# Kernel tuning notes

Measured on AMD Instinct MI355X. Metric: run time of the kernel, lower is better.

## Reference

```python
import jax, jax.numpy as jnp
import numpy as np

NF = 16            # num_frequencies
S = 2              # scale_factor
MAX_STD = 0.5
POS_LIMIT = 1.0


def setup_inputs() -> dict:
    key = jax.random.key(0)
    ks = jax.random.split(key, 8)
    B, G, H, W = 16, 256, 128, 128
    hidden, base = 1024, 256
    in_dim = (G + 2 * NF + 1) * S * S  # 4624
    # xavier-uniform-like scales
    lim1 = float(np.sqrt(6.0 / (hidden + in_dim)))
    lim2 = float(np.sqrt(6.0 / (base + hidden)))
    return {
        "position": jax.random.uniform(ks[0], (B, 4), dtype=jnp.float32),
        "gestalt": jax.random.normal(ks[1], (B, G), dtype=jnp.float32),
        "mask": jax.random.uniform(ks[2], (B, 1, H, W), dtype=jnp.float32),
        "depth": jax.random.normal(ks[3], (B, 1, H, W), dtype=jnp.float32),
        "weight1": jax.random.uniform(ks[4], (hidden, in_dim), minval=-lim1, maxval=lim1, dtype=jnp.float32),
        "bias1": jnp.zeros((hidden,), dtype=jnp.float32),
        "weight2": jax.random.uniform(ks[5], (base, hidden), minval=-lim2, maxval=lim2, dtype=jnp.float32),
        "bias2": jnp.zeros((base,), dtype=jnp.float32),
    }


def reference(position, gestalt, mask, depth, weight1, bias1, weight2, bias2):
    B, _, H, W = mask.shape
    # positional grids in [-1, 1], shapes (1,1,H,W)
    gx = (jnp.arange(W, dtype=jnp.float32) / (W - 1)) * 2 - 1
    gy = (jnp.arange(H, dtype=jnp.float32) / (H - 1)) * 2 - 1
    grid_y, grid_x = jnp.meshgrid(gy, gx, indexing="ij")
    grid_x = grid_x[None, None]
    grid_y = grid_y[None, None]

    x = jnp.clip(position[:, 0], -POS_LIMIT, POS_LIMIT)[:, None, None, None]
    y = jnp.clip(position[:, 1], -POS_LIMIT, POS_LIMIT)[:, None, None, None]
    min_std = 1.0 / min(H, W)
    std = 0.1 / jnp.clip(position[:, 3], min_std, MAX_STD)[:, None, None, None]
    std_y = std
    std_x = std * (W / H)

    half_pi = jnp.float32(np.pi / 2)
    ngx = (grid_x - x) * std_x * half_pi  # (B,1,H,W)
    ngy = (grid_y - y) * std_y * half_pi
    freqs = (2.0 ** jnp.arange(NF, dtype=jnp.float32))[None, :, None, None]
    cos_x = jnp.cos(ngx * freqs)  # (B,NF,H,W)
    cos_y = jnp.cos(ngy * freqs)
    # interleave: [cx0, cy0, cx1, cy1, ...]
    embedding = jnp.stack([cos_x, cos_y], axis=2).reshape(B, 2 * NF, H, W)

    inp = jnp.concatenate(
        [gestalt[:, :, None, None] * mask, embedding * mask, depth * mask], axis=1
    )  # (B,C,H,W)
    C = inp.shape[1]
    # space-to-depth patchify
    p = inp.reshape(B, C, H // S, S, W // S, S)
    p = p.transpose(0, 2, 4, 1, 3, 5).reshape(B * (H // S) * (W // S), C * S * S)

    h = p @ weight1.T + bias1
    h = h * jax.nn.sigmoid(h)  # SiLU
    o = h @ weight2.T + bias2
    return o.reshape(B, H // S, W // S, -1).transpose(0, 3, 1, 2)
```

## Files before the change

kernel.cpp:

```cpp
#include <hip/hip_runtime.h>
#include <cstdio>


#define NFREQ 16
#define BB 16
#define G 256
#define KIN 1156
#define K1 144
#define STAGE_U16 12800
#define NSTAGE 6

typedef unsigned short u16;
using bf16x8 = __bf16 __attribute__((ext_vector_type(8)));
using f32x16 = float __attribute__((ext_vector_type(16)));
using f32x4  = float __attribute__((ext_vector_type(4)));

__device__ __forceinline__ u16 f2bf(float f) {
  unsigned u = __float_as_uint(f);
  u += 0x7fffu + ((u >> 16) & 1u);
  return (u16)(u >> 16);
}
__device__ __forceinline__ unsigned pk2(float a, float b) {
  return (unsigned)f2bf(a) | ((unsigned)f2bf(b) << 16);
}
__device__ __forceinline__ unsigned pk2f(float a, float b) {
  unsigned ua = __float_as_uint(a) + 0x8000u;
  unsigned ub = __float_as_uint(b) + 0x8000u;
  return __builtin_amdgcn_perm(ub, ua, 0x07060302u);
}
__device__ __forceinline__ float silu(float h) {
  float e = __builtin_amdgcn_exp2f(h * -1.44269504088896f);
  return h * __builtin_amdgcn_rcpf(1.f + e);
}
__device__ __forceinline__ void gl_lds16(const u16* g, u16* l) {
  __builtin_amdgcn_global_load_lds(
      (const __attribute__((address_space(1))) void*)g,
      (__attribute__((address_space(3))) void*)l, 16, 0, 0);
}

__global__ void k_pre(const float* __restrict__ pos,
                      const float* __restrict__ gestalt,
                      const float* __restrict__ w1,
                      const float* __restrict__ w2,
                      const float* __restrict__ bias1,
                      float* __restrict__ cosx, float* __restrict__ cosy,
                      u16* __restrict__ B1F, u16* __restrict__ W2F) {
  const int bid = blockIdx.x;
  const int t = threadIdx.x;

  if (bid < 1024) {
    __shared__ float w1row[KIN];
    __shared__ float gestT[G * 17];
    __shared__ float psum[256];
    __shared__ float wg[64];
    const int n = bid;
    const float b1v = bias1[n];
#pragma unroll
    for (int i = t; i < KIN; i += 256) w1row[i] = w1[(size_t)n * KIN + i];
#pragma unroll
    for (int i = t; i < BB * G; i += 256) {
      int bb = i >> 8, c = i & 255;
      gestT[c * 17 + bb] = gestalt[i];
    }
    __syncthreads();
    {
      int bb = t & 15, j = (t >> 4) & 3, q = t >> 6;
      float acc = 0.f;
#pragma unroll 8
      for (int c = q * 64; c < q * 64 + 64; ++c)
        acc += gestT[c * 17 + bb] * w1row[4 * c + j];
      psum[t] = acc;
    }
    __syncthreads();
    if (t < 64) {
      int bb = t >> 2, j = t & 3;
      wg[t] = psum[j * 16 + bb] + psum[64 + j * 16 + bb] +
              psum[128 + j * 16 + bb] + psum[192 + j * 16 + bb];
    }
    __syncthreads();
    const int ch = n >> 5, l31n = n & 31;
    for (int c = t; c < BB * (K1 / 8); c += 256) {
      int bb = c / 18, kc = c - bb * 18;
      int k0 = kc * 8;
      float v[8];
#pragma unroll
      for (int i = 0; i < 8; ++i) {
        int k = k0 + i;
        float vv;
        if (k < 64)       vv = w1row[1024 + 8 * (k >> 2) + (k & 3)];
        else if (k < 128) { int kk = k - 64; vv = w1row[1024 + 8 * (kk >> 2) + 4 + (kk & 3)]; }
        else if (k < 132) vv = wg[bb * 4 + (k - 128)];
        else if (k < 136) vv = w1row[1152 + (k - 132)];
        else if (k == 136) vv = b1v;
        else              vv = 0.f;
        v[i] = vv;
      }
      uint4 u;
      u.x = pk2(v[0], v[1]); u.y = pk2(v[2], v[3]);
      u.z = pk2(v[4], v[5]); u.w = pk2(v[6], v[7]);
      size_t idx0 = ((((size_t)bb * 32 + ch) * 9 + (kc >> 1)) * 64 +
                     (kc & 1) * 32 + l31n) * 8;
      *(uint4*)(B1F + idx0) = u;
    }
  } else if (bid < 1152) {
    int e8 = (bid - 1024) * 256 + t;
    int lane = e8 & 63;
    int ct   = (e8 >> 6) & 7;
    int kc   = e8 >> 9;
    int n2 = ct * 32 + (lane & 31);
    int k2 = kc * 16 + (lane >> 5) * 8;
    const float* src = w2 + (size_t)n2 * 1024 + k2;
    uint4 u;
    u.x = pk2(src[0], src[1]); u.y = pk2(src[2], src[3]);
    u.z = pk2(src[4], src[5]); u.w = pk2(src[6], src[7]);
    *(uint4*)(W2F + (size_t)e8 * 8) = u;
  } else {
    int idx = (bid - 1152) * 256 + t;
    int table = idx >> 15;
    int rem = idx & 32767;
    int b = rem >> 11;
    int f = (rem >> 7) & 15;
    int c = rem & 127;
    float p0 = pos[b * 4 + 0];
    float p1 = pos[b * 4 + 1];
    float p3 = pos[b * 4 + 3];
    float x = fminf(fmaxf(p0, -1.f), 1.f);
    float y = fminf(fmaxf(p1, -1.f), 1.f);
    float stdv = 0.1f / fminf(fmaxf(p3, 0.0078125f), 0.5f);
    const float half_pi = 1.57079632679489661923f;
    float g = ((float)c / 127.0f) * 2.0f - 1.0f;
    float ng = (table == 0) ? ((g - x) * stdv) * half_pi
                            : ((g - y) * stdv) * half_pi;
    float freq = (float)(1 << f);
    float val = cosf(ng * freq);
    if (table == 0) cosx[(b * NFREQ + f) * 128 + c] = val;
    else            cosy[(b * NFREQ + f) * 128 + c] = val;
  }
}


__device__ __forceinline__ f32x16 mfma_bf16(bf16x8 a, bf16x8 b, f32x16 c) {
  return __builtin_amdgcn_mfma_f32_32x32x16_bf16(a, b, c, 0, 0, 0);
}

__device__ __forceinline__ void gemm1(const u16* afb, const bf16x8* bfr, int lane8,
                                      const f32x16& ZERO, f32x16& a1a, f32x16& a1b) {
  bf16x8 af0 = *(const bf16x8*)(afb + 0 * 512 + lane8);
  bf16x8 af1 = *(const bf16x8*)(afb + 1 * 512 + lane8);
  a1a = mfma_bf16(af0, bfr[0], ZERO);
  a1b = mfma_bf16(af1, bfr[1], ZERO);
#pragma unroll
  for (int ks = 1; ks < 4; ++ks) {
    bf16x8 afa = *(const bf16x8*)(afb + (2 * ks) * 512 + lane8);
    bf16x8 afc = *(const bf16x8*)(afb + (2 * ks + 1) * 512 + lane8);
    a1a = mfma_bf16(afa, bfr[2 * ks], a1a);
    a1b = mfma_bf16(afc, bfr[2 * ks + 1], a1b);
  }
  bf16x8 af8 = *(const bf16x8*)(afb + 8 * 512 + lane8);
  a1a = mfma_bf16(af8, bfr[8], a1a);
}

__device__ __forceinline__ void gemm2(const u16* wfb, int lane8,
                                      bf16x8 fA, bf16x8 fB, f32x16* acc2) {
#pragma unroll
  for (int ct = 0; ct < 8; ++ct) {
    bf16x8 wf = *(const bf16x8*)(wfb + ct * 512 + lane8);
    acc2[ct] = mfma_bf16(fA, wf, acc2[ct]);
  }
#pragma unroll
  for (int ct = 0; ct < 8; ++ct) {
    bf16x8 wf = *(const bf16x8*)(wfb + 4096 + ct * 512 + lane8);
    acc2[ct] = mfma_bf16(fB, wf, acc2[ct]);
  }
}

__device__ __forceinline__ void silupack(const f32x16& a1a, const f32x16& a1b,
                                         bf16x8& fragA, bf16x8& fragB) {
  unsigned d[8];
#pragma unroll
  for (int q = 0; q < 4; ++q) {
    float s0 = silu(a1a[4 * q + 0] + a1b[4 * q + 0]);
    float s1 = silu(a1a[4 * q + 1] + a1b[4 * q + 1]);
    float s2 = silu(a1a[4 * q + 2] + a1b[4 * q + 2]);
    float s3 = silu(a1a[4 * q + 3] + a1b[4 * q + 3]);
    d[2 * q]     = pk2f(s0, s1);
    d[2 * q + 1] = pk2f(s2, s3);
  }
  unsigned e0 = d[0], e1 = d[2];
  unsigned e2 = d[1], e3 = d[3];
  unsigned e4 = d[4], e5 = d[6];
  unsigned e6 = d[5], e7 = d[7];
  asm("v_permlane32_swap_b32 %0, %1" : "+v"(e0), "+v"(e1));
  asm("v_permlane32_swap_b32 %0, %1" : "+v"(e2), "+v"(e3));
  asm("v_permlane32_swap_b32 %0, %1" : "+v"(e4), "+v"(e5));
  asm("v_permlane32_swap_b32 %0, %1" : "+v"(e6), "+v"(e7));
  uint4 fav, fbv;
  fav.x = e0; fav.y = e2; fav.z = e1; fav.w = e3;
  fbv.x = e4; fbv.y = e6; fbv.z = e5; fbv.w = e7;
  fragA = __builtin_bit_cast(bf16x8, fav);
  fragB = __builtin_bit_cast(bf16x8, fbv);
}

__global__ __launch_bounds__(512, 2) void k_main(
    const u16* __restrict__ B1F, const u16* __restrict__ W2F,
    const float* __restrict__ mask, const float* __restrict__ depth,
    const float* __restrict__ cosx, const float* __restrict__ cosy,
    const float* __restrict__ bias2, float* __restrict__ out)
{
  __shared__ __align__(16) u16 sbuf[NSTAGE * STAGE_U16];
  float* stg = (float*)sbuf;

  const int tid = threadIdx.x;
  const int w = tid >> 6;
  const int lane = tid & 63;
  const int lane8 = lane * 8;
  const int l31 = lane & 31;
  const int lhi = lane >> 5;
  const int bswz = (blockIdx.x & 7) * 32 + (blockIdx.x >> 3);
  const int r0 = bswz * 256;
  const int b = r0 >> 12;
  const int oy0 = (r0 >> 6) & 63;

  {
    const float4* cx4 = (const float4*)(cosx + (size_t)b * 2048);
    ((float4*)stg)[tid] = cx4[tid];
    if (tid < 128)
      stg[2048 + tid] = cosy[((size_t)b * 16 + (tid >> 3)) * 128 + 2 * oy0 + (tid & 7)];
    if (tid < 256) {
      ((float4*)(stg + 2176))[tid] = ((const float4*)(mask  + ((size_t)b * 128 + 2 * oy0) * 128))[tid];
      ((float4*)(stg + 3200))[tid] = ((const float4*)(depth + ((size_t)b * 128 + 2 * oy0) * 128))[tid];
    }
  }
  __syncthreads();

  bf16x8 bfr[9];
  {
    const int r = w * 32 + l31;
    const int oyl = r >> 6, ox = r & 63;
    float m[4], dd[4];
#pragma unroll
    for (int j = 0; j < 4; ++j) {
      int sy = j >> 1, sx = j & 1;
      float mv = stg[2176 + (2 * oyl + sy) * 128 + 2 * ox + sx];
      m[j] = mv;
      dd[j] = stg[3200 + (2 * oyl + sy) * 128 + 2 * ox + sx] * mv;
    }
#pragma unroll
    for (int ks = 0; ks < 9; ++ks) {
      const int k0 = ks * 16 + lhi * 8;
      unsigned dwords[4];
#pragma unroll
      for (int h = 0; h < 4; ++h) {
        float v[2];
#pragma unroll
        for (int p = 0; p < 2; ++p) {
          const int k = k0 + 2 * h + p;
          float vv;
          if (k < 64) {
            const int f = k >> 2, j = k & 3;
            vv = m[j] * stg[f * 128 + 2 * ox + (j & 1)];
          } else if (k < 128) {
            const int kk = k - 64, f = kk >> 2, j = kk & 3;
            vv = m[j] * stg[2048 + f * 8 + 2 * oyl + (j >> 1)];
          } else if (k < 132) {
            vv = m[k - 128];
          } else if (k < 136) {
            vv = dd[k - 132];
          } else if (k == 136) {
            vv = 1.0f;
          } else {
            vv = 0.f;
          }
          v[p] = vv;
        }
        dwords[h] = pk2(v[0], v[1]);
      }
      uint4 u; u.x = dwords[0]; u.y = dwords[1]; u.z = dwords[2]; u.w = dwords[3];
      bfr[ks] = __builtin_bit_cast(bf16x8, u);
    }
  }
  __syncthreads();

  f32x16 acc2[8];
#pragma unroll
  for (int c = 0; c < 8; ++c)
#pragma unroll
    for (int i = 0; i < 16; ++i) acc2[c][i] = 0.f;

  f32x16 ZERO;
#pragma unroll
  for (int i = 0; i < 16; ++i) ZERO[i] = 0.f;

  const u16* apre = B1F + (size_t)b * 32 * 4608 + lane8;
  const u16* wpre = W2F + lane8;

  auto prefetchP = [&](u16* dst) {
    gl_lds16(apre + w * 512, dst + w * 512);
    if (w == 7) gl_lds16(apre + 8 * 512, dst + 8 * 512);
    gl_lds16(wpre + w * 512, dst + (9 + w) * 512);
    gl_lds16(wpre + (8 + w) * 512, dst + (17 + w) * 512);
    apre += 4608; wpre += 8192;
  };

  prefetchP(sbuf);
  prefetchP(sbuf + STAGE_U16);
  prefetchP(sbuf + 2 * STAGE_U16);

  bf16x8 fragA, fragB;

  {
    if (w == 7) asm volatile("s_waitcnt vmcnt(4)" ::: "memory");
    else        asm volatile("s_waitcnt vmcnt(3)" ::: "memory");
    __builtin_amdgcn_s_barrier();
    asm volatile("" ::: "memory");
    __builtin_amdgcn_sched_barrier(0);
    prefetchP(sbuf + 3 * STAGE_U16);

    f32x16 a1a, a1b;
    __builtin_amdgcn_s_setprio(1);
    gemm1(sbuf, bfr, lane8, ZERO, a1a, a1b);
    __builtin_amdgcn_s_setprio(0);
    silupack(a1a, a1b, fragA, fragB);
  }

  int st = 1;
  int stw = 4;
  for (int ch = 1; ch < 32; ++ch) {
    if (!(ch & 1)) {
      if (ch == 30) asm volatile("s_waitcnt vmcnt(0)" ::: "memory");
      else if (w == 7) asm volatile("s_waitcnt vmcnt(4)" ::: "memory");
      else             asm volatile("s_waitcnt vmcnt(3)" ::: "memory");
      __builtin_amdgcn_s_barrier();
      asm volatile("" ::: "memory");
      __builtin_amdgcn_sched_barrier(0);
    }
    if (ch + 3 < 32) prefetchP(sbuf + stw * STAGE_U16);
    stw = (stw + 1 == NSTAGE) ? 0 : stw + 1;

    const u16* afb  = sbuf + st * STAGE_U16;
    const int  stp  = (st == 0) ? NSTAGE - 1 : st - 1;
    const u16* wfbp = sbuf + stp * STAGE_U16 + 4608;

    f32x16 a1a, a1b;
    __builtin_amdgcn_s_setprio(1);
    gemm1(afb, bfr, lane8, ZERO, a1a, a1b);
    gemm2(wfbp, lane8, fragA, fragB, acc2);
    __builtin_amdgcn_s_setprio(0);

    silupack(a1a, a1b, fragA, fragB);
    st = (st + 1 == NSTAGE) ? 0 : st + 1;
  }

  gemm2(sbuf + 1 * STAGE_U16 + 4608, lane8, fragA, fragB, acc2);

#pragma unroll
  for (int ct = 0; ct < 8; ++ct) {
    const int n2 = ct * 32 + l31;
    const float b2 = bias2[n2];
    float* ob = out + ((size_t)b * 256 + n2) * 4096;
#pragma unroll
    for (int q = 0; q < 4; ++q) {
      const int rl = w * 32 + 8 * q + 4 * lhi;
      const int oy = oy0 + (rl >> 6);
      const int ox = rl & 63;
      f32x4 v;
      v[0] = acc2[ct][4 * q + 0] + b2;
      v[1] = acc2[ct][4 * q + 1] + b2;
      v[2] = acc2[ct][4 * q + 2] + b2;
      v[3] = acc2[ct][4 * q + 3] + b2;
      *(f32x4*)(ob + oy * 64 + ox) = v;
    }
  }
}


extern "C" void kernel_launch(void* const* d_in, const int* in_sizes, int n_in,
                              void* d_out, int out_size, void* d_ws, size_t ws_size,
                              hipStream_t stream) {
  const float* pos     = (const float*)d_in[0];
  const float* gestalt = (const float*)d_in[1];
  const float* mask    = (const float*)d_in[2];
  const float* depth   = (const float*)d_in[3];
  const float* w1      = (const float*)d_in[4];
  const float* bias1   = (const float*)d_in[5];
  const float* w2      = (const float*)d_in[6];
  const float* bias2   = (const float*)d_in[7];
  float* out = (float*)d_out;

  const size_t NEED = 131072u + 131072u + 4718592u + 524288u;
  if (ws_size < NEED) {
    fprintf(stderr, "[kernel] ws_size=%zu < needed %zu — skipping launches\n",
            ws_size, NEED);
    return;
  }
  char* ws = (char*)d_ws;
  float* cosx = (float*)(ws);
  float* cosy = (float*)(ws + 131072);
  u16*   B1F  = (u16*)(ws + 262144);
  u16*   W2F  = (u16*)(ws + 262144 + 4718592);

  k_pre<<<1408, 256, 0, stream>>>(pos, gestalt, w1, w2, bias1, cosx, cosy, B1F, W2F);
  k_main<<<256, 512, 0, stream>>>(B1F, W2F, mask, depth, cosx, cosy, bias2, out);
}
```

Measured before the change: 156.5 us.

## Split batch-invariant W1 fragments from per-batch part, stagger SiLU across wave groups

After: 149.9 us, median of 3. -4.2%, faster.

```diff
diff --git a/kernel.cpp b/kernel.cpp
--- a/kernel.cpp
+++ b/kernel.cpp
@@ -44,7 +44,8 @@
                       const float* __restrict__ w2,
                       const float* __restrict__ bias1,
                       float* __restrict__ cosx, float* __restrict__ cosy,
-                      u16* __restrict__ B1F, u16* __restrict__ W2F) {
+                      u16* __restrict__ B1FS, u16* __restrict__ B1FB,
+                      u16* __restrict__ W2F) {
   const int bid = blockIdx.x;
   const int t = threadIdx.x;
 
@@ -79,8 +80,10 @@
     }
     __syncthreads();
     const int ch = n >> 5, l31n = n & 31;
-    for (int c = t; c < BB * (K1 / 8); c += 256) {
-      int bb = c / 18, kc = c - bb * 18;
+    if (t < 48) {
+      int bb, kc;
+      if (t < 16) { bb = 0; kc = t; }
+      else        { bb = (t - 16) >> 1; kc = 16 + ((t - 16) & 1); }
       int k0 = kc * 8;
       float v[8];
 #pragma unroll
@@ -98,9 +101,13 @@
       uint4 u;
       u.x = pk2(v[0], v[1]); u.y = pk2(v[2], v[3]);
       u.z = pk2(v[4], v[5]); u.w = pk2(v[6], v[7]);
-      size_t idx0 = ((((size_t)bb * 32 + ch) * 9 + (kc >> 1)) * 64 +
-                     (kc & 1) * 32 + l31n) * 8;
-      *(uint4*)(B1F + idx0) = u;
+      if (kc < 16) {
+        size_t idx0 = (((size_t)ch * 8 + (kc >> 1)) * 64 + (kc & 1) * 32 + l31n) * 8;
+        *(uint4*)(B1FS + idx0) = u;
+      } else {
+        size_t idx0 = (((size_t)bb * 32 + ch) * 64 + (kc - 16) * 32 + l31n) * 8;
+        *(uint4*)(B1FB + idx0) = u;
+      }
     }
   } else if (bid < 1152) {
     int e8 = (bid - 1024) * 256 + t;
@@ -202,7 +209,8 @@
 }
 
 __global__ __launch_bounds__(512, 2) void k_main(
-    const u16* __restrict__ B1F, const u16* __restrict__ W2F,
+    const u16* __restrict__ B1FS, const u16* __restrict__ B1FB,
+    const u16* __restrict__ W2F,
     const float* __restrict__ mask, const float* __restrict__ depth,
     const float* __restrict__ cosx, const float* __restrict__ cosy,
     const float* __restrict__ bias2, float* __restrict__ out)
@@ -216,6 +224,7 @@
   const int lane8 = lane * 8;
   const int l31 = lane & 31;
   const int lhi = lane >> 5;
+  const bool gA = (w < 4);
   const int bswz = (blockIdx.x & 7) * 32 + (blockIdx.x >> 3);
   const int r0 = bswz * 256;
   const int b = r0 >> 12;
@@ -291,15 +300,16 @@
 #pragma unroll
   for (int i = 0; i < 16; ++i) ZERO[i] = 0.f;
 
-  const u16* apre = B1F + (size_t)b * 32 * 4608 + lane8;
-  const u16* wpre = W2F + lane8;
+  const u16* apre_s = B1FS + lane8;
+  const u16* apre_b = B1FB + (size_t)b * 16384 + lane8;
+  const u16* wpre   = W2F + lane8;
 
   auto prefetchP = [&](u16* dst) {
-    gl_lds16(apre + w * 512, dst + w * 512);
-    if (w == 7) gl_lds16(apre + 8 * 512, dst + 8 * 512);
+    gl_lds16(apre_s + w * 512, dst + w * 512);
+    if (w == 7) gl_lds16(apre_b, dst + 8 * 512);
     gl_lds16(wpre + w * 512, dst + (9 + w) * 512);
     gl_lds16(wpre + (8 + w) * 512, dst + (17 + w) * 512);
-    apre += 4608; wpre += 8192;
+    apre_s += 4096; apre_b += 512; wpre += 8192;
   };
 
   prefetchP(sbuf);
@@ -307,6 +317,7 @@
   prefetchP(sbuf + 2 * STAGE_U16);
 
   bf16x8 fragA, fragB;
+  f32x16 pa, pb;
 
   {
     if (w == 7) asm volatile("s_waitcnt vmcnt(4)" ::: "memory");
@@ -320,7 +331,11 @@
     __builtin_amdgcn_s_setprio(1);
     gemm1(sbuf, bfr, lane8, ZERO, a1a, a1b);
     __builtin_amdgcn_s_setprio(0);
-    silupack(a1a, a1b, fragA, fragB);
+    if (gA) {
+      silupack(a1a, a1b, fragA, fragB);
+    } else {
+      pa = a1a; pb = a1b;
+    }
   }
 
   int st = 1;
@@ -341,16 +356,26 @@
     const int  stp  = (st == 0) ? NSTAGE - 1 : st - 1;
     const u16* wfbp = sbuf + stp * STAGE_U16 + 4608;
 
-    f32x16 a1a, a1b;
-    __builtin_amdgcn_s_setprio(1);
-    gemm1(afb, bfr, lane8, ZERO, a1a, a1b);
-    gemm2(wfbp, lane8, fragA, fragB, acc2);
-    __builtin_amdgcn_s_setprio(0);
-
-    silupack(a1a, a1b, fragA, fragB);
+    if (gA) {
+      f32x16 a1a, a1b;
+      __builtin_amdgcn_s_setprio(1);
+      gemm1(afb, bfr, lane8, ZERO, a1a, a1b);
+      gemm2(wfbp, lane8, fragA, fragB, acc2);
+      __builtin_amdgcn_s_setprio(0);
+      silupack(a1a, a1b, fragA, fragB);
+    } else {
+      silupack(pa, pb, fragA, fragB);
+      f32x16 a1a, a1b;
+      __builtin_amdgcn_s_setprio(1);
+      gemm1(afb, bfr, lane8, ZERO, a1a, a1b);
+      gemm2(wfbp, lane8, fragA, fragB, acc2);
+      __builtin_amdgcn_s_setprio(0);
+      pa = a1a; pb = a1b;
+    }
     st = (st + 1 == NSTAGE) ? 0 : st + 1;
   }
 
+  if (!gA) silupack(pa, pb, fragA, fragB);
   gemm2(sbuf + 1 * STAGE_U16 + 4608, lane8, fragA, fragB, acc2);
 
 #pragma unroll
@@ -387,7 +412,7 @@
   const float* bias2   = (const float*)d_in[7];
   float* out = (float*)d_out;
 
-  const size_t NEED = 131072u + 131072u + 4718592u + 524288u;
+  const size_t NEED = 131072u + 131072u + 262144u + 524288u + 524288u;
   if (ws_size < NEED) {
     fprintf(stderr, "[kernel] ws_size=%zu < needed %zu — skipping launches\n",
             ws_size, NEED);
@@ -396,9 +421,12 @@
   char* ws = (char*)d_ws;
   float* cosx = (float*)(ws);
   float* cosy = (float*)(ws + 131072);
-  u16*   B1F  = (u16*)(ws + 262144);
-  u16*   W2F  = (u16*)(ws + 262144 + 4718592);
-
-  k_pre<<<1408, 256, 0, stream>>>(pos, gestalt, w1, w2, bias1, cosx, cosy, B1F, W2F);
-  k_main<<<256, 512, 0, stream>>>(B1F, W2F, mask, depth, cosx, cosy, bias2, out);
-}
+  u16*   B1FS = (u16*)(ws + 262144);
+  u16*   B1FB = (u16*)(ws + 262144 + 262144);
+  u16*   W2F  = (u16*)(ws + 262144 + 262144 + 524288);
+
+  k_pre<<<1408, 256, 0, stream>>>(pos, gestalt, w1, w2, bias1, cosx, cosy,
+                                  B1FS, B1FB, W2F);
+  k_main<<<256, 512, 0, stream>>>(B1FS, B1FB, W2F, mask, depth, cosx, cosy,
+                                  bias2, out);
+}
```
